# Kernel optimization log

Hardware: AMD Instinct MI355X
Metric: run time of the kernel (lower is better)

The kernel has to match this reference:

```python
import jax, jax.numpy as jnp
import numpy as np

N = 6144      # total atoms
F = 128       # hidden_dim
NB = 48       # number of molecules (batch segments)
LONG_RANGE_SCALE = 1.0


def setup_inputs() -> dict:
    key = jax.random.key(0)
    ks = jax.random.split(key, 16)
    s = 1.0 / np.sqrt(F)
    return {
        "h0": jax.random.normal(ks[0], (N, F), jnp.float32),
        "h1": jax.random.normal(ks[1], (N, 3, F), jnp.float32),
        "pos": jax.random.normal(ks[2], (N, 3), jnp.float32),
        "batch": jnp.sort(jax.random.randint(ks[3], (N,), 0, NB)),
        "qW1": jax.random.normal(ks[4], (F, F // 2), jnp.float32) * s,
        "qb1": jnp.zeros((F // 2,), jnp.float32),
        "qW2": jax.random.normal(ks[5], (F // 2, 1), jnp.float32) * s,
        "qb2": jnp.zeros((1,), jnp.float32),
        "cW1": jax.random.normal(ks[6], (F, F // 2), jnp.float32) * s,
        "cb1": jnp.zeros((F // 2,), jnp.float32),
        "cW2": jax.random.normal(ks[7], (F // 2, 1), jnp.float32) * s,
        "cb2": jnp.zeros((1,), jnp.float32),
        "muW": jax.random.normal(ks[8], (F, 1), jnp.float32) * s,
    }


def reference(h0, h1, pos, batch, qW1, qb1, qW2, qb2, cW1, cb1, cW2, cb2, muW):
    n = pos.shape[0]
    # pairwise geometry
    batch_mask = batch[:, None] == batch[None, :]                 # (N,N) bool
    diff = pos[:, None, :] - pos[None, :, :]                      # (N,N,3)
    dist_sq = jnp.sum(diff * diff, axis=-1)                       # (N,N)
    dist = jnp.sqrt(dist_sq + 1e-8)
    valid = batch_mask & ~jnp.eye(n, dtype=bool)
    validf = valid.astype(dist.dtype)

    energy = jnp.zeros((), dist.dtype)

    # --- Coulomb (use_charge) ---
    q = jax.nn.silu(h0 @ qW1 + qb1) @ qW2 + qb2                   # (N,1)
    q_sum = jax.ops.segment_sum(q, batch, num_segments=NB)        # (NB,1)
    cnt = jax.ops.segment_sum(jnp.ones((n, 1), q.dtype), batch, num_segments=NB)
    q_mean = q_sum / jnp.maximum(cnt, 1.0)                        # scatter_mean
    q = q - q_mean[batch]                                         # per-molecule neutrality
    qq = q @ q.T                                                  # (N,N)
    f_taper = 1.0 - jnp.exp(-0.5 * dist)
    E_coul = jnp.sum(qq / dist * f_taper * validf)
    energy = energy + 0.5 * E_coul * 14.399

    # --- van der Waals (use_vdw) ---
    c6 = jax.nn.softplus(jax.nn.silu(h0 @ cW1 + cb1) @ cW2 + cb2)  # (N,1), >0
    c6_ij = jnp.sqrt(c6 @ c6.T)                                    # (N,N)
    r6 = dist_sq ** 3
    E_vdw = -jnp.sum(c6_ij / (r6 + 20.0) * validf)
    energy = energy + 0.5 * E_vdw

    # --- dipole-dipole (use_dipole) ---
    mu = (h1 @ muW)[..., 0]                                        # (N,3)
    mu_dot_mu = mu @ mu.T                                          # (N,N)
    n_ij = diff / (dist[..., None] + 1e-8)                         # (N,N,3)
    mu_dot_n_i = jnp.einsum("id,ijd->ij", mu, n_ij)
    mu_dot_n_j = jnp.einsum("jd,ijd->ij", mu, n_ij)
    inv_r3 = 1.0 / (dist_sq * dist + 10.0)
    E_dip = jnp.sum((mu_dot_mu - 3.0 * mu_dot_n_i * mu_dot_n_j) * inv_r3 * validf)
    energy = energy + 0.5 * E_dip

    return energy * LONG_RANGE_SCALE
```

## Files before the change

kernel.cpp:

```cpp
#include <hip/hip_runtime.h>
#include <math.h>

#define F 128
#define H 64
#define NBMOL 48
#define ATB 16
#define CAP 256
#define SPLIT 16

__device__ __forceinline__ float silu_f(float x) {
    return x / (1.0f + __expf(-x));
}
__device__ __forceinline__ float softplus_f(float x) {
    return fmaxf(x, 0.0f) + log1pf(__expf(-fabsf(x)));
}
__device__ __forceinline__ float frcp(float x) {
    return __builtin_amdgcn_rcpf(x);
}

__global__ __launch_bounds__(256, 2) void k_atom(
    const float* __restrict__ h0, const float* __restrict__ h1,
    const int* __restrict__ batch,
    const float* __restrict__ qW1, const float* __restrict__ qb1,
    const float* __restrict__ qW2, const float* __restrict__ qb2,
    const float* __restrict__ cW1, const float* __restrict__ cb1,
    const float* __restrict__ cW2, const float* __restrict__ cb2,
    const float* __restrict__ muW,
    float* __restrict__ q_raw, float* __restrict__ sqc6,
    float* __restrict__ mu,
    int* __restrict__ segstart, int* __restrict__ segend,
    float* __restrict__ out, int N)
{
    const int tid = threadIdx.x;
    if (blockIdx.x == 0 && tid == 0) out[0] = 0.0f;

    const int lane = tid & 63;
    const int w = tid >> 6;
    const int net = w & 1;
    const int grp = w >> 1;
    int a0 = __builtin_amdgcn_readfirstlane(blockIdx.x * ATB + grp * 8);

    const float* __restrict__ W1 = net ? cW1 : qW1;
    const float* __restrict__ b1 = net ? cb1 : qb1;
    const float* __restrict__ W2 = net ? cW2 : qW2;

    float wreg[F];
    #pragma unroll
    for (int f = 0; f < F; ++f) wreg[f] = W1[f * H + lane];

    const float4* __restrict__ r[8];
    #pragma unroll
    for (int a = 0; a < 8; ++a)
        r[a] = (const float4*)(h0 + (size_t)min(a0 + a, N - 1) * F);

    float acc[8];
    {
        float b = b1[lane];
        #pragma unroll
        for (int a = 0; a < 8; ++a) acc[a] = b;
    }

    #pragma unroll
    for (int fb = 0; fb < F / 4; ++fb) {
        #pragma unroll
        for (int a = 0; a < 8; ++a) {
            float4 x = r[a][fb];
            acc[a] = fmaf(x.x, wreg[4 * fb + 0],
                     fmaf(x.y, wreg[4 * fb + 1],
                     fmaf(x.z, wreg[4 * fb + 2],
                     fmaf(x.w, wreg[4 * fb + 3], acc[a]))));
        }
    }

    const float w2 = W2[lane];
    float v[8];
    #pragma unroll
    for (int a = 0; a < 8; ++a) v[a] = silu_f(acc[a]) * w2;

    #pragma unroll
    for (int off = 32; off > 0; off >>= 1) {
        #pragma unroll
        for (int a = 0; a < 8; ++a) v[a] += __shfl_xor(v[a], off);
    }

    const float b2v = net ? cb2[0] : qb2[0];
    #pragma unroll
    for (int a = 0; a < 8; ++a) {
        if (lane == a) {
            int i = a0 + a;
            if (i < N) {
                float s = v[a] + b2v;
                if (net == 0) {
                    q_raw[i] = s;
                    int b = batch[i];
                    if (i == 0 || batch[i - 1] != b) segstart[b] = i;
                    if (i == N - 1 || batch[i + 1] != b) segend[b] = i + 1;
                } else {
                    sqc6[i] = sqrtf(softplus_f(s));
                }
            }
        }
    }

    const int hw = lane >> 5;
    const int hl = lane & 31;
    const float4 mw4 = ((const float4*)muW)[hl];
    const int rbase = blockIdx.x * (ATB * 3) + w * 12;
    #pragma unroll
    for (int s = 0; s < 6; ++s) {
        int row = rbase + s * 2 + hw;
        if (row < 3 * N) {
            const float4* rp = (const float4*)(h1 + (size_t)row * F);
            float4 hv = rp[hl];
            float pm = fmaf(hv.x, mw4.x, fmaf(hv.y, mw4.y,
                       fmaf(hv.z, mw4.z, hv.w * mw4.w)));
            #pragma unroll
            for (int off = 16; off > 0; off >>= 1) pm += __shfl_xor(pm, off);
            if (hl == 0) mu[row] = pm;
        }
    }
}

__global__ __launch_bounds__(256) void k_pair(
    const float* __restrict__ pos,
    const float* __restrict__ q_raw, const float* __restrict__ sqc6,
    const float* __restrict__ mu,
    const int* __restrict__ segstart, const int* __restrict__ segend,
    float* __restrict__ out)
{
    const int b = blockIdx.x;
    const int s = blockIdx.y;
    const int tid = threadIdx.x;
    const int st = segstart[b];
    const int n = segend[b] - st;

    __shared__ float sq[CAP], sc[CAP], sp[3 * CAP], sm[3 * CAP];
    __shared__ float red[4];

    float e_c = 0.f, e_v = 0.f, e_d = 0.f;

    if (n > 1 && n <= CAP) {
        float part = 0.f;
        for (int k = tid; k < n; k += 256) {
            float qv = q_raw[st + k];
            sq[k] = qv; part += qv;
            sc[k] = sqc6[st + k];
        }
        for (int k = tid; k < 3 * n; k += 256) {
            sp[k] = pos[3 * st + k];
            sm[k] = mu[3 * st + k];
        }
        #pragma unroll
        for (int off = 32; off > 0; off >>= 1) part += __shfl_xor(part, off);
        if ((tid & 63) == 0) red[tid >> 6] = part;
        __syncthreads();
        const float mean = (red[0] + red[1] + red[2] + red[3]) / (float)n;

        const int r = tid >> 4;
        const int c = tid & 15;
        for (int il = s + SPLIT * r; il < n; il += SPLIT * 16) {
            const float qi = sq[il] - mean;
            const float sci = sc[il];
            const float xi = sp[3 * il], yi = sp[3 * il + 1], zi = sp[3 * il + 2];
            const float mxi = sm[3 * il], myi = sm[3 * il + 1], mzi = sm[3 * il + 2];
            for (int jl = c; jl < n; jl += 16) {
                if (jl == il) continue;
                float dx = xi - sp[3 * jl], dy = yi - sp[3 * jl + 1],
                      dz = zi - sp[3 * jl + 2];
                float ds0 = fmaf(dx, dx, fmaf(dy, dy, dz * dz));
                float d = sqrtf(ds0 + 1e-8f);
                float inv_d = frcp(d);
                float qj = sq[jl] - mean;
                e_c = fmaf(qi * qj * inv_d, 1.0f - __expf(-0.5f * d), e_c);
                float r6 = ds0 * ds0 * ds0;
                e_v = fmaf(sci * sc[jl], frcp(r6 + 20.0f), e_v);
                float smx = sm[3 * jl], smy = sm[3 * jl + 1], smz = sm[3 * jl + 2];
                float mdm = fmaf(mxi, smx, fmaf(myi, smy, mzi * smz));
                float mdni = fmaf(mxi, dx, fmaf(myi, dy, mzi * dz)) * inv_d;
                float mdnj = fmaf(smx, dx, fmaf(smy, dy, smz * dz)) * inv_d;
                e_d = fmaf(mdm - 3.0f * mdni * mdnj,
                           frcp(fmaf(ds0, d, 10.0f)), e_d);
            }
        }
    } else if (n > CAP) {
        float part = 0.f;
        for (int k = tid; k < n; k += 256) part += q_raw[st + k];
        #pragma unroll
        for (int off = 32; off > 0; off >>= 1) part += __shfl_xor(part, off);
        if ((tid & 63) == 0) red[tid >> 6] = part;
        __syncthreads();
        const float mean = (red[0] + red[1] + red[2] + red[3]) / (float)n;
        const int r = tid >> 4, c = tid & 15;
        for (int j0 = 0; j0 < n; j0 += CAP) {
            const int chunk = min(CAP, n - j0);
            __syncthreads();
            for (int k = tid; k < chunk; k += 256) {
                sq[k] = q_raw[st + j0 + k];
                sc[k] = sqc6[st + j0 + k];
            }
            for (int k = tid; k < 3 * chunk; k += 256) {
                sp[k] = pos[3 * (st + j0) + k];
                sm[k] = mu[3 * (st + j0) + k];
            }
            __syncthreads();
            for (int il = s + SPLIT * r; il < n; il += SPLIT * 16) {
                const int i = st + il;
                const float qi = q_raw[i] - mean;
                const float sci = sqc6[i];
                const float xi = pos[i * 3], yi = pos[i * 3 + 1], zi = pos[i * 3 + 2];
                const float mxi = mu[i * 3], myi = mu[i * 3 + 1], mzi = mu[i * 3 + 2];
                for (int jl = c; jl < chunk; jl += 16) {
                    if (j0 + jl == il) continue;
                    float dx = xi - sp[3 * jl], dy = yi - sp[3 * jl + 1],
                          dz = zi - sp[3 * jl + 2];
                    float ds0 = fmaf(dx, dx, fmaf(dy, dy, dz * dz));
                    float d = sqrtf(ds0 + 1e-8f);
                    float inv_d = frcp(d);
                    float qj = sq[jl] - mean;
                    e_c = fmaf(qi * qj * inv_d, 1.0f - __expf(-0.5f * d), e_c);
                    float r6 = ds0 * ds0 * ds0;
                    e_v = fmaf(sci * sc[jl], frcp(r6 + 20.0f), e_v);
                    float smx = sm[3 * jl], smy = sm[3 * jl + 1], smz = sm[3 * jl + 2];
                    float mdm = fmaf(mxi, smx, fmaf(myi, smy, mzi * smz));
                    float mdni = fmaf(mxi, dx, fmaf(myi, dy, mzi * dz)) * inv_d;
                    float mdnj = fmaf(smx, dx, fmaf(smy, dy, smz * dz)) * inv_d;
                    e_d = fmaf(mdm - 3.0f * mdni * mdnj,
                               frcp(fmaf(ds0, d, 10.0f)), e_d);
                }
            }
        }
    }

    float vv = fmaf(7.1995f, e_c, fmaf(-0.5f, e_v, 0.5f * e_d));
    #pragma unroll
    for (int off = 32; off > 0; off >>= 1) vv += __shfl_xor(vv, off);
    __syncthreads();
    if ((tid & 63) == 0) red[tid >> 6] = vv;
    __syncthreads();
    if (tid == 0) atomicAdd(out, red[0] + red[1] + red[2] + red[3]);
}

extern "C" void kernel_launch(void* const* d_in, const int* in_sizes, int n_in,
                              void* d_out, int out_size, void* d_ws, size_t ws_size,
                              hipStream_t stream) {
    const float* h0  = (const float*)d_in[0];
    const float* h1  = (const float*)d_in[1];
    const float* pos = (const float*)d_in[2];
    const int*   batch = (const int*)d_in[3];
    const float* qW1 = (const float*)d_in[4];
    const float* qb1 = (const float*)d_in[5];
    const float* qW2 = (const float*)d_in[6];
    const float* qb2 = (const float*)d_in[7];
    const float* cW1 = (const float*)d_in[8];
    const float* cb1 = (const float*)d_in[9];
    const float* cW2 = (const float*)d_in[10];
    const float* cb2 = (const float*)d_in[11];
    const float* muW = (const float*)d_in[12];
    float* out = (float*)d_out;
    const int N = in_sizes[0] / F;

    float* ws = (float*)d_ws;
    int* segstart = (int*)ws;
    int* segend   = (int*)(ws + 48);
    float* q_raw = ws + 128;
    float* sqc6  = q_raw + N;
    float* mu    = sqc6 + N;

    int nblk = (N + ATB - 1) / ATB;
    k_atom<<<nblk, 256, 0, stream>>>(h0, h1, batch, qW1, qb1, qW2, qb2,
                                     cW1, cb1, cW2, cb2, muW,
                                     q_raw, sqc6, mu, segstart, segend,
                                     out, N);
    k_pair<<<dim3(NBMOL, SPLIT), 256, 0, stream>>>(pos, q_raw, sqc6, mu,
                                                   segstart, segend, out);
}
```

Baseline: 128.8 us.

## Restructure per-atom MLP kernel: transpose weights, map threads to hidden units

Measured after the change: 136.6 us. +6.1%, slower.

```diff
diff --git a/kernel.cpp b/kernel.cpp
--- a/kernel.cpp
+++ b/kernel.cpp
@@ -4,7 +4,7 @@
 #define F 128
 #define H 64
 #define NBMOL 48
-#define ATB 16
+#define BATOMS 4
 #define CAP 256
 #define SPLIT 16
 
@@ -17,108 +17,109 @@
 __device__ __forceinline__ float frcp(float x) {
     return __builtin_amdgcn_rcpf(x);
 }
-
-__global__ __launch_bounds__(256, 2) void k_atom(
+__device__ __forceinline__ float dot4(float4 a, float4 b) {
+    return fmaf(a.x, b.x, fmaf(a.y, b.y, fmaf(a.z, b.z, a.w * b.w)));
+}
+
+__global__ __launch_bounds__(256) void k_prep(
+    const float* __restrict__ qW1, const float* __restrict__ cW1,
+    float* __restrict__ wtq, float* __restrict__ wtc,
+    float* __restrict__ out)
+{
+    int idx = blockIdx.x * 256 + threadIdx.x;
+    if (idx == 0) out[0] = 0.0f;
+    int net = idx >> 13;
+    int e = idx & 8191;
+    int h = e >> 7, f = e & 127;
+    const float* src = net ? cW1 : qW1;
+    float* dst = net ? wtc : wtq;
+    dst[e] = src[f * H + h];
+}
+
+__global__ __launch_bounds__(256, 4) void k_atom(
     const float* __restrict__ h0, const float* __restrict__ h1,
     const int* __restrict__ batch,
-    const float* __restrict__ qW1, const float* __restrict__ qb1,
+    const float* __restrict__ wtq, const float* __restrict__ qb1,
     const float* __restrict__ qW2, const float* __restrict__ qb2,
-    const float* __restrict__ cW1, const float* __restrict__ cb1,
+    const float* __restrict__ wtc, const float* __restrict__ cb1,
     const float* __restrict__ cW2, const float* __restrict__ cb2,
     const float* __restrict__ muW,
     float* __restrict__ q_raw, float* __restrict__ sqc6,
     float* __restrict__ mu,
-    int* __restrict__ segstart, int* __restrict__ segend,
-    float* __restrict__ out, int N)
+    int* __restrict__ segstart, int* __restrict__ segend, int N)
 {
     const int tid = threadIdx.x;
-    if (blockIdx.x == 0 && tid == 0) out[0] = 0.0f;
-
+    const int h  = tid >> 2;
+    const int al = tid & 3;
+    const int i  = min(blockIdx.x * BATOMS + al, N - 1);
+
+    const float4* __restrict__ xr = (const float4*)(h0 + (size_t)i * F);
+    const float4* __restrict__ wq = (const float4*)(wtq + (size_t)h * F);
+    const float4* __restrict__ wc = (const float4*)(wtc + (size_t)h * F);
+
+    float zq = qb1[h];
+    float zc = cb1[h];
+    #pragma unroll 8
+    for (int fb = 0; fb < F / 4; ++fb) {
+        float4 x = xr[fb];
+        float4 a = wq[fb];
+        float4 b = wc[fb];
+        zq += dot4(x, a);
+        zc += dot4(x, b);
+    }
+
+    float vq = silu_f(zq) * qW2[h];
+    float vc = silu_f(zc) * cW2[h];
+
+    #pragma unroll
+    for (int off = 4; off < 64; off <<= 1) {
+        vq += __shfl_xor(vq, off);
+        vc += __shfl_xor(vc, off);
+    }
+
+    __shared__ float redw[4][2][4];
+    __shared__ float dred[1];
+    const int w = tid >> 6;
     const int lane = tid & 63;
-    const int w = tid >> 6;
-    const int net = w & 1;
-    const int grp = w >> 1;
-    int a0 = __builtin_amdgcn_readfirstlane(blockIdx.x * ATB + grp * 8);
-
-    const float* __restrict__ W1 = net ? cW1 : qW1;
-    const float* __restrict__ b1 = net ? cb1 : qb1;
-    const float* __restrict__ W2 = net ? cW2 : qW2;
-
-    float wreg[F];
-    #pragma unroll
-    for (int f = 0; f < F; ++f) wreg[f] = W1[f * H + lane];
-
-    const float4* __restrict__ r[8];
-    #pragma unroll
-    for (int a = 0; a < 8; ++a)
-        r[a] = (const float4*)(h0 + (size_t)min(a0 + a, N - 1) * F);
-
-    float acc[8];
-    {
-        float b = b1[lane];
-        #pragma unroll
-        for (int a = 0; a < 8; ++a) acc[a] = b;
-    }
-
-    #pragma unroll
-    for (int fb = 0; fb < F / 4; ++fb) {
-        #pragma unroll
-        for (int a = 0; a < 8; ++a) {
-            float4 x = r[a][fb];
-            acc[a] = fmaf(x.x, wreg[4 * fb + 0],
-                     fmaf(x.y, wreg[4 * fb + 1],
-                     fmaf(x.z, wreg[4 * fb + 2],
-                     fmaf(x.w, wreg[4 * fb + 3], acc[a]))));
-        }
-    }
-
-    const float w2 = W2[lane];
-    float v[8];
-    #pragma unroll
-    for (int a = 0; a < 8; ++a) v[a] = silu_f(acc[a]) * w2;
-
-    #pragma unroll
-    for (int off = 32; off > 0; off >>= 1) {
-        #pragma unroll
-        for (int a = 0; a < 8; ++a) v[a] += __shfl_xor(v[a], off);
-    }
-
-    const float b2v = net ? cb2[0] : qb2[0];
-    #pragma unroll
-    for (int a = 0; a < 8; ++a) {
-        if (lane == a) {
-            int i = a0 + a;
-            if (i < N) {
-                float s = v[a] + b2v;
-                if (net == 0) {
-                    q_raw[i] = s;
-                    int b = batch[i];
-                    if (i == 0 || batch[i - 1] != b) segstart[b] = i;
-                    if (i == N - 1 || batch[i + 1] != b) segend[b] = i + 1;
-                } else {
-                    sqc6[i] = sqrtf(softplus_f(s));
-                }
-            }
-        }
-    }
-
-    const int hw = lane >> 5;
-    const int hl = lane & 31;
-    const float4 mw4 = ((const float4*)muW)[hl];
-    const int rbase = blockIdx.x * (ATB * 3) + w * 12;
-    #pragma unroll
-    for (int s = 0; s < 6; ++s) {
-        int row = rbase + s * 2 + hw;
+    if (lane < 4) {
+        redw[w][0][lane] = vq;
+        redw[w][1][lane] = vc;
+    }
+    __syncthreads();
+
+    if (tid < 8) {
+        int a = tid & 3, net = tid >> 2;
+        int ia = blockIdx.x * BATOMS + a;
+        if (ia < N) {
+            float z = redw[0][net][a] + redw[1][net][a] +
+                      redw[2][net][a] + redw[3][net][a];
+            if (net == 0) {
+                float qv = z + qb2[0];
+                q_raw[ia] = qv;
+                int b = batch[ia];
+                if (ia == 0 || batch[ia - 1] != b) segstart[b] = ia;
+                if (ia == N - 1 || batch[ia + 1] != b) segend[b] = ia + 1;
+            } else {
+                sqc6[ia] = sqrtf(softplus_f(z + cb2[0]));
+            }
+        }
+    }
+
+    const int slot = tid >> 4;
+    const int l = tid & 15;
+    if (slot < 3 * BATOMS) {
+        int row = blockIdx.x * (3 * BATOMS) + slot;
         if (row < 3 * N) {
             const float4* rp = (const float4*)(h1 + (size_t)row * F);
-            float4 hv = rp[hl];
-            float pm = fmaf(hv.x, mw4.x, fmaf(hv.y, mw4.y,
-                       fmaf(hv.z, mw4.z, hv.w * mw4.w)));
+            const float4* mp = (const float4*)muW;
+            float pm = dot4(rp[2 * l], mp[2 * l]) +
+                       dot4(rp[2 * l + 1], mp[2 * l + 1]);
             #pragma unroll
-            for (int off = 16; off > 0; off >>= 1) pm += __shfl_xor(pm, off);
-            if (hl == 0) mu[row] = pm;
-        }
-    }
+            for (int off = 1; off < 16; off <<= 1) pm += __shfl_xor(pm, off);
+            if (l == 0) mu[row] = pm;
+        }
+    }
+    (void)dred;
 }
 
 __global__ __launch_bounds__(256) void k_pair(
@@ -265,12 +266,15 @@
     float* q_raw = ws + 128;
     float* sqc6  = q_raw + N;
     float* mu    = sqc6 + N;
-
-    int nblk = (N + ATB - 1) / ATB;
-    k_atom<<<nblk, 256, 0, stream>>>(h0, h1, batch, qW1, qb1, qW2, qb2,
-                                     cW1, cb1, cW2, cb2, muW,
-                                     q_raw, sqc6, mu, segstart, segend,
-                                     out, N);
+    float* wtq   = mu + 3 * N;
+    float* wtc   = wtq + F * H;
+
+    k_prep<<<64, 256, 0, stream>>>(qW1, cW1, wtq, wtc, out);
+
+    int nblk = (N + BATOMS - 1) / BATOMS;
+    k_atom<<<nblk, 256, 0, stream>>>(h0, h1, batch, wtq, qb1, qW2, qb2,
+                                     wtc, cb1, cW2, cb2, muW,
+                                     q_raw, sqc6, mu, segstart, segend, N);
     k_pair<<<dim3(NBMOL, SPLIT), 256, 0, stream>>>(pos, q_raw, sqc6, mu,
                                                    segstart, segend, out);
 }
```

## Tile atom MLP through swizzled LDS and split hidden dim across blocks

Applied to the files above, without the earlier changes.

Result: faster. 113.9 us (median of 2 runs) (-11.6%).

```diff
diff --git a/kernel.cpp b/kernel.cpp
--- a/kernel.cpp
+++ b/kernel.cpp
@@ -3,8 +3,9 @@
 
 #define F 128
 #define H 64
+#define HH 32
+#define AT 64
 #define NBMOL 48
-#define ATB 16
 #define CAP 256
 #define SPLIT 16
 
@@ -17,116 +18,130 @@
 __device__ __forceinline__ float frcp(float x) {
     return __builtin_amdgcn_rcpf(x);
 }
-
-__global__ __launch_bounds__(256, 2) void k_atom(
+__device__ __forceinline__ float dot4(float4 a, float4 b) {
+    return fmaf(a.x, b.x, fmaf(a.y, b.y, fmaf(a.z, b.z, a.w * b.w)));
+}
+
+__global__ __launch_bounds__(256, 4) void k_atom(
     const float* __restrict__ h0, const float* __restrict__ h1,
     const int* __restrict__ batch,
     const float* __restrict__ qW1, const float* __restrict__ qb1,
-    const float* __restrict__ qW2, const float* __restrict__ qb2,
+    const float* __restrict__ qW2,
     const float* __restrict__ cW1, const float* __restrict__ cb1,
-    const float* __restrict__ cW2, const float* __restrict__ cb2,
+    const float* __restrict__ cW2,
     const float* __restrict__ muW,
-    float* __restrict__ q_raw, float* __restrict__ sqc6,
+    float* __restrict__ part,
     float* __restrict__ mu,
     int* __restrict__ segstart, int* __restrict__ segend,
-    float* __restrict__ out, int N)
+    float* __restrict__ out, int N, int nmlp, int ndip)
 {
+    __shared__ float4 sW4[HH * 32];
+    __shared__ float4 sX4[AT * 32];
+    __shared__ float red[4][AT];
+
+    const int b = blockIdx.x;
     const int tid = threadIdx.x;
-    if (blockIdx.x == 0 && tid == 0) out[0] = 0.0f;
-
-    const int lane = tid & 63;
-    const int w = tid >> 6;
-    const int net = w & 1;
-    const int grp = w >> 1;
-    int a0 = __builtin_amdgcn_readfirstlane(blockIdx.x * ATB + grp * 8);
-
-    const float* __restrict__ W1 = net ? cW1 : qW1;
-    const float* __restrict__ b1 = net ? cb1 : qb1;
-    const float* __restrict__ W2 = net ? cW2 : qW2;
-
-    float wreg[F];
-    #pragma unroll
-    for (int f = 0; f < F; ++f) wreg[f] = W1[f * H + lane];
-
-    const float4* __restrict__ r[8];
-    #pragma unroll
-    for (int a = 0; a < 8; ++a)
-        r[a] = (const float4*)(h0 + (size_t)min(a0 + a, N - 1) * F);
-
-    float acc[8];
-    {
-        float b = b1[lane];
+
+    if (b < nmlp) {
+        const int tile  = b >> 2;
+        const int net   = b & 1;
+        const int hhalf = (b >> 1) & 1;
+        const float* __restrict__ W1 = net ? cW1 : qW1;
+        const float* __restrict__ b1 = net ? cb1 : qb1;
+        const float* __restrict__ W2 = net ? cW2 : qW2;
+
+        for (int idx = tid; idx < HH * F; idx += 256) {
+            int f = idx >> 5;
+            int hh = idx & 31;
+            float val = W1[f * H + hhalf * HH + hh];
+            int f4 = f >> 2, fi = f & 3;
+            ((float*)&sW4[hh * 32 + (f4 ^ ((hh >> 1) & 7))])[fi] = val;
+        }
+        const float4* __restrict__ h0v = (const float4*)h0;
+        for (int idx = tid; idx < AT * 32; idx += 256) {
+            int a = idx >> 5, f4 = idx & 31;
+            int row = min(tile * AT + a, N - 1);
+            sX4[a * 32 + (f4 ^ ((a >> 2) & 7))] = h0v[(size_t)row * 32 + f4];
+        }
+        __syncthreads();
+
+        const int ag = tid & 15;
+        const int hg = tid >> 4;
+        const int swx = ag & 7;
+        const int sww = hg & 7;
+        const int h0i = hhalf * HH + 2 * hg;
+
+        float z[4][2];
+        {
+            float b0 = b1[h0i], b1v = b1[h0i + 1];
+            #pragma unroll
+            for (int j = 0; j < 4; ++j) { z[j][0] = b0; z[j][1] = b1v; }
+        }
+
+        #pragma unroll 4
+        for (int f4 = 0; f4 < 32; ++f4) {
+            float4 w0 = sW4[(2 * hg) * 32 + (f4 ^ sww)];
+            float4 w1 = sW4[(2 * hg + 1) * 32 + (f4 ^ sww)];
+            #pragma unroll
+            for (int j = 0; j < 4; ++j) {
+                float4 x = sX4[(4 * ag + j) * 32 + (f4 ^ swx)];
+                z[j][0] += dot4(x, w0);
+                z[j][1] += dot4(x, w1);
+            }
+        }
+
+        const float w2a = W2[h0i], w2b = W2[h0i + 1];
+        float p[4];
         #pragma unroll
-        for (int a = 0; a < 8; ++a) acc[a] = b;
-    }
-
-    #pragma unroll
-    for (int fb = 0; fb < F / 4; ++fb) {
+        for (int j = 0; j < 4; ++j)
+            p[j] = fmaf(silu_f(z[j][0]), w2a, silu_f(z[j][1]) * w2b);
+
         #pragma unroll
-        for (int a = 0; a < 8; ++a) {
-            float4 x = r[a][fb];
-            acc[a] = fmaf(x.x, wreg[4 * fb + 0],
-                     fmaf(x.y, wreg[4 * fb + 1],
-                     fmaf(x.z, wreg[4 * fb + 2],
-                     fmaf(x.w, wreg[4 * fb + 3], acc[a]))));
-        }
-    }
-
-    const float w2 = W2[lane];
-    float v[8];
-    #pragma unroll
-    for (int a = 0; a < 8; ++a) v[a] = silu_f(acc[a]) * w2;
-
-    #pragma unroll
-    for (int off = 32; off > 0; off >>= 1) {
-        #pragma unroll
-        for (int a = 0; a < 8; ++a) v[a] += __shfl_xor(v[a], off);
-    }
-
-    const float b2v = net ? cb2[0] : qb2[0];
-    #pragma unroll
-    for (int a = 0; a < 8; ++a) {
-        if (lane == a) {
-            int i = a0 + a;
-            if (i < N) {
-                float s = v[a] + b2v;
-                if (net == 0) {
-                    q_raw[i] = s;
-                    int b = batch[i];
-                    if (i == 0 || batch[i - 1] != b) segstart[b] = i;
-                    if (i == N - 1 || batch[i + 1] != b) segend[b] = i + 1;
-                } else {
-                    sqc6[i] = sqrtf(softplus_f(s));
-                }
-            }
-        }
-    }
-
-    const int hw = lane >> 5;
-    const int hl = lane & 31;
-    const float4 mw4 = ((const float4*)muW)[hl];
-    const int rbase = blockIdx.x * (ATB * 3) + w * 12;
-    #pragma unroll
-    for (int s = 0; s < 6; ++s) {
-        int row = rbase + s * 2 + hw;
+        for (int j = 0; j < 4; ++j) {
+            p[j] += __shfl_xor(p[j], 16);
+            p[j] += __shfl_xor(p[j], 32);
+        }
+        const int wv = tid >> 6, lane = tid & 63;
+        if (lane < 16) {
+            #pragma unroll
+            for (int j = 0; j < 4; ++j) red[wv][4 * lane + j] = p[j];
+        }
+        __syncthreads();
+        if (tid < AT) {
+            float s = red[0][tid] + red[1][tid] + red[2][tid] + red[3][tid];
+            int atom = tile * AT + tid;
+            if (atom < N) part[(size_t)(net * 2 + hhalf) * N + atom] = s;
+        }
+    } else if (b < nmlp + ndip) {
+        const int slot = tid >> 4;
+        const int l = tid & 15;
+        int row = (b - nmlp) * 16 + slot;
         if (row < 3 * N) {
             const float4* rp = (const float4*)(h1 + (size_t)row * F);
-            float4 hv = rp[hl];
-            float pm = fmaf(hv.x, mw4.x, fmaf(hv.y, mw4.y,
-                       fmaf(hv.z, mw4.z, hv.w * mw4.w)));
+            const float4* mp = (const float4*)muW;
+            float pm = dot4(rp[2 * l], mp[2 * l]) +
+                       dot4(rp[2 * l + 1], mp[2 * l + 1]);
             #pragma unroll
-            for (int off = 16; off > 0; off >>= 1) pm += __shfl_xor(pm, off);
-            if (hl == 0) mu[row] = pm;
+            for (int off = 1; off < 16; off <<= 1) pm += __shfl_xor(pm, off);
+            if (l == 0) mu[row] = pm;
+        }
+    } else {
+        if (tid == 0) out[0] = 0.0f;
+        for (int i = tid; i < N; i += 256) {
+            int bb = batch[i];
+            if (i == 0 || batch[i - 1] != bb) segstart[bb] = i;
+            if (i == N - 1 || batch[i + 1] != bb) segend[bb] = i + 1;
         }
     }
 }
 
 __global__ __launch_bounds__(256) void k_pair(
     const float* __restrict__ pos,
-    const float* __restrict__ q_raw, const float* __restrict__ sqc6,
+    const float* __restrict__ part,
     const float* __restrict__ mu,
+    const float* __restrict__ qb2, const float* __restrict__ cb2,
     const int* __restrict__ segstart, const int* __restrict__ segend,
-    float* __restrict__ out)
+    float* __restrict__ out, int N)
 {
     const int b = blockIdx.x;
     const int s = blockIdx.y;
@@ -134,25 +149,32 @@
     const int st = segstart[b];
     const int n = segend[b] - st;
 
+    const float* __restrict__ p0 = part;
+    const float* __restrict__ p1 = part + N;
+    const float* __restrict__ p2 = part + 2 * (size_t)N;
+    const float* __restrict__ p3 = part + 3 * (size_t)N;
+    const float qb2v = qb2[0], cb2v = cb2[0];
+
     __shared__ float sq[CAP], sc[CAP], sp[3 * CAP], sm[3 * CAP];
     __shared__ float red[4];
 
     float e_c = 0.f, e_v = 0.f, e_d = 0.f;
 
     if (n > 1 && n <= CAP) {
-        float part = 0.f;
+        float partsum = 0.f;
         for (int k = tid; k < n; k += 256) {
-            float qv = q_raw[st + k];
-            sq[k] = qv; part += qv;
-            sc[k] = sqc6[st + k];
+            float qv = p0[st + k] + p1[st + k] + qb2v;
+            sq[k] = qv; partsum += qv;
+            sc[k] = sqrtf(softplus_f(p2[st + k] + p3[st + k] + cb2v));
         }
         for (int k = tid; k < 3 * n; k += 256) {
             sp[k] = pos[3 * st + k];
             sm[k] = mu[3 * st + k];
         }
         #pragma unroll
-        for (int off = 32; off > 0; off >>= 1) part += __shfl_xor(part, off);
-        if ((tid & 63) == 0) red[tid >> 6] = part;
+        for (int off = 32; off > 0; off >>= 1)
+            partsum += __shfl_xor(partsum, off);
+        if ((tid & 63) == 0) red[tid >> 6] = partsum;
         __syncthreads();
         const float mean = (red[0] + red[1] + red[2] + red[3]) / (float)n;
 
@@ -183,11 +205,13 @@
             }
         }
     } else if (n > CAP) {
-        float part = 0.f;
-        for (int k = tid; k < n; k += 256) part += q_raw[st + k];
+        float partsum = 0.f;
+        for (int k = tid; k < n; k += 256)
+            partsum += p0[st + k] + p1[st + k] + qb2v;
         #pragma unroll
-        for (int off = 32; off > 0; off >>= 1) part += __shfl_xor(part, off);
-        if ((tid & 63) == 0) red[tid >> 6] = part;
+        for (int off = 32; off > 0; off >>= 1)
+            partsum += __shfl_xor(partsum, off);
+        if ((tid & 63) == 0) red[tid >> 6] = partsum;
         __syncthreads();
         const float mean = (red[0] + red[1] + red[2] + red[3]) / (float)n;
         const int r = tid >> 4, c = tid & 15;
@@ -195,8 +219,9 @@
             const int chunk = min(CAP, n - j0);
             __syncthreads();
             for (int k = tid; k < chunk; k += 256) {
-                sq[k] = q_raw[st + j0 + k];
-                sc[k] = sqc6[st + j0 + k];
+                int j = st + j0 + k;
+                sq[k] = p0[j] + p1[j] + qb2v;
+                sc[k] = sqrtf(softplus_f(p2[j] + p3[j] + cb2v));
             }
             for (int k = tid; k < 3 * chunk; k += 256) {
                 sp[k] = pos[3 * (st + j0) + k];
@@ -205,8 +230,8 @@
             __syncthreads();
             for (int il = s + SPLIT * r; il < n; il += SPLIT * 16) {
                 const int i = st + il;
-                const float qi = q_raw[i] - mean;
-                const float sci = sqc6[i];
+                const float qi = p0[i] + p1[i] + qb2v - mean;
+                const float sci = sqrtf(softplus_f(p2[i] + p3[i] + cb2v));
                 const float xi = pos[i * 3], yi = pos[i * 3 + 1], zi = pos[i * 3 + 2];
                 const float mxi = mu[i * 3], myi = mu[i * 3 + 1], mzi = mu[i * 3 + 2];
                 for (int jl = c; jl < chunk; jl += 16) {
@@ -262,15 +287,18 @@
     float* ws = (float*)d_ws;
     int* segstart = (int*)ws;
     int* segend   = (int*)(ws + 48);
-    float* q_raw = ws + 128;
-    float* sqc6  = q_raw + N;
-    float* mu    = sqc6 + N;
-
-    int nblk = (N + ATB - 1) / ATB;
-    k_atom<<<nblk, 256, 0, stream>>>(h0, h1, batch, qW1, qb1, qW2, qb2,
-                                     cW1, cb1, cW2, cb2, muW,
-                                     q_raw, sqc6, mu, segstart, segend,
-                                     out, N);
-    k_pair<<<dim3(NBMOL, SPLIT), 256, 0, stream>>>(pos, q_raw, sqc6, mu,
-                                                   segstart, segend, out);
-}
+    float* part = ws + 128;
+    float* mu   = part + 4 * (size_t)N;
+
+    const int ntile = (N + AT - 1) / AT;
+    const int nmlp = 4 * ntile;
+    const int ndip = (3 * N + 15) / 16;
+    const int grid = nmlp + ndip + 1;
+
+    k_atom<<<grid, 256, 0, stream>>>(h0, h1, batch, qW1, qb1, qW2,
+                                     cW1, cb1, cW2, muW,
+                                     part, mu, segstart, segend, out,
+                                     N, nmlp, ndip);
+    k_pair<<<dim3(NBMOL, SPLIT), 256, 0, stream>>>(pos, part, mu, qb2, cb2,
+                                                   segstart, segend, out, N);
+}
```
